# Kernel tuning notes

Measured on AMD Instinct MI355X. Metric: run time of the kernel, lower is better.

The kernel has to match this reference:

```python
import jax, jax.numpy as jnp
import numpy as np
from jax import lax

B, T, CIN, COUT, FACTOR = 2, 2048, 512, 512, 2
KUP = FACTOR * 2          # transposed-conv kernel
PUP = FACTOR // 2         # transposed-conv padding
KR, PR = 7, 3             # refine conv kernel/padding
EPS = 1e-5


def _ste(x, q):
    # straight-through estimator: forward = q, backward = identity
    return x + lax.stop_gradient(q - x)


def act_quant(x):
    # BitNet b1.58 per-token int8 absmax quant; x is (B, C, L), quant over C
    scale = 127.0 / jnp.maximum(jnp.max(jnp.abs(x), axis=1, keepdims=True), 1e-5)
    q = jnp.clip(jnp.round(x * scale), -128, 127) / scale
    return _ste(x, q)


def weight_quant(w):
    # ternary {-1,0,1} * scale, scale = mean |w|
    scale = 1.0 / jnp.maximum(jnp.mean(jnp.abs(w)), 1e-5)
    q = jnp.clip(jnp.round(w * scale), -1, 1) / scale
    return _ste(w, q)


def bit_conv1d(x, w, b, pad):
    # x: (B,C,L), w: (Cout,Cin,K) torch layout
    y = lax.conv_general_dilated(
        act_quant(x), weight_quant(w), window_strides=(1,),
        padding=[(pad, pad)], dimension_numbers=('NCH', 'OIH', 'NCH'))
    return y + b[None, :, None]


def bit_conv_transpose1d(x, w, b, stride, pad):
    # x: (B,Cin,L), w: (Cin,Cout,K) torch ConvTranspose1d layout
    k = w.shape[2]
    y = lax.conv_general_dilated(
        act_quant(x), jnp.flip(weight_quant(w), 2), window_strides=(1,),
        padding=[(k - 1 - pad, k - 1 - pad)], lhs_dilation=(stride,),
        dimension_numbers=('NCH', 'IOH', 'NCH'))
    return y + b[None, :, None]


def setup_inputs() -> dict:
    key = jax.random.key(0)
    ks = jax.random.split(key, 7)
    s_up = 1.0 / np.sqrt(CIN * KUP)
    s_r = 1.0 / np.sqrt(COUT * KR)
    return {
        'x': jax.random.normal(ks[0], (B, T, CIN), jnp.float32),
        'w_up': jax.random.normal(ks[1], (CIN, COUT, KUP), jnp.float32) * s_up,
        'b_up': jnp.zeros((COUT,), jnp.float32),
        'w_r1': jax.random.normal(ks[2], (COUT, COUT, KR), jnp.float32) * s_r,
        'b_r1': jnp.zeros((COUT,), jnp.float32),
        'w_r2': jax.random.normal(ks[3], (COUT, COUT, KR), jnp.float32) * s_r,
        'b_r2': jnp.zeros((COUT,), jnp.float32),
        'ln_w': jnp.ones((COUT,), jnp.float32),
        'ln_b': jnp.zeros((COUT,), jnp.float32),
    }


def reference(x, w_up, b_up, w_r1, b_r1, w_r2, b_r2, ln_w, ln_b):
    h = jnp.swapaxes(x, 1, 2)                                  # (B,Cin,T)
    h = bit_conv_transpose1d(h, w_up, b_up, FACTOR, PUP)       # (B,Cout,factor*T)
    r = bit_conv1d(h, w_r1, b_r1, PR)
    r = jax.nn.silu(r)
    r = bit_conv1d(r, w_r2, b_r2, PR)
    h = h + r
    h = jnp.swapaxes(h, 1, 2)                                  # (B,L,Cout)
    mu = jnp.mean(h, axis=-1, keepdims=True)
    var = jnp.mean(jnp.square(h - mu), axis=-1, keepdims=True)
    return (h - mu) * lax.rsqrt(var + EPS) * ln_w + ln_b
```

## Files before the change

### kernel.cpp

```cpp
#include <hip/hip_runtime.h>
#include <hip/hip_bf16.h>
#include <cstdint>
#include <cstddef>


#define B_ 2
#define T_ 2048
#define L_ 4096
#define C_ 512

static constexpr int NUP = 512 * 512 * 4;
static constexpr int NR  = 512 * 512 * 7;

using v4i  = __attribute__((ext_vector_type(4))) int;
using v16i = __attribute__((ext_vector_type(16))) int;

__device__ __forceinline__ void gl16(const void* g, void* l) {
  __builtin_amdgcn_global_load_lds((const __attribute__((address_space(1))) unsigned int*)g,
                                   (__attribute__((address_space(3))) unsigned int*)l,
                                   16, 0, 0);
}


__device__ inline float block_reduce_sum_256(float v) {
  #pragma unroll
  for (int off = 32; off > 0; off >>= 1) v += __shfl_down(v, off, 64);
  __shared__ float s[4];
  __syncthreads();
  if ((threadIdx.x & 63) == 0) s[threadIdx.x >> 6] = v;
  __syncthreads();
  return (s[0] + s[1]) + (s[2] + s[3]);
}

__global__ void abssum3_partial(const float* __restrict__ w0, const float* __restrict__ w1,
                                const float* __restrict__ w2, float* __restrict__ partial) {
  int y = blockIdx.y;
  const float* w = (y == 0) ? w0 : (y == 1) ? w1 : w2;
  int n = (y == 0) ? NUP : NR;
  int idx = blockIdx.x * 256 + threadIdx.x;
  float s = 0.f;
  for (int i = idx; i < n; i += gridDim.x * 256) s += fabsf(w[i]);
  s = block_reduce_sum_256(s);
  if (threadIdx.x == 0) partial[y * 256 + blockIdx.x] = s;
}

__global__ void abssum3_final(const float* __restrict__ partial, float* __restrict__ out) {
  int y = blockIdx.x;
  float v = partial[y * 256 + threadIdx.x];
  v = block_reduce_sum_256(v);
  if (threadIdx.x == 0) out[y] = v;
}

__global__ void tern_all_kernel(const float* __restrict__ wu, const float* __restrict__ w1,
                                const float* __restrict__ w2, int8_t* __restrict__ ou,
                                int8_t* __restrict__ o1, int8_t* __restrict__ o2,
                                const float* __restrict__ wsum) {
  int y = blockIdx.y;
  int idx = blockIdx.x * 256 + threadIdx.x;
  if (y == 0) {
    if (idx >= NUP) return;
    float mean = wsum[0] * (1.0f / (float)NUP);
    float scale = 1.0f / fmaxf(mean, 1e-5f);
    float t = rintf(wu[idx] * scale);
    t = fminf(fmaxf(t, -1.f), 1.f);
    int ci = idx >> 11;
    int co = (idx >> 2) & 511;
    int k = idx & 3;
    int ptap = (k == 3) ? 0 : (k == 1) ? 1 : (k == 2) ? 2 : 3;
    ou[(((size_t)ptap * 32 + (ci >> 4)) * 512 + co) * 16 + (ci & 15)] = (int8_t)t;
  } else {
    if (idx >= NR) return;
    const float* w = (y == 1) ? w1 : w2;
    int8_t* o = (y == 1) ? o1 : o2;
    float mean = wsum[y] * (1.0f / (float)NR);
    float scale = 1.0f / fmaxf(mean, 1e-5f);
    float t = rintf(w[idx] * scale);
    t = fminf(fmaxf(t, -1.f), 1.f);
    int co = idx / 3584;
    int rem = idx - co * 3584;
    int ci = rem / 7;
    int k = rem - ci * 7;
    o[(((size_t)k * 32 + (ci >> 4)) * 512 + co) * 16 + (ci & 15)] = (int8_t)t;
  }
}

__global__ void act_quant_kernel(const float* __restrict__ x, int8_t* __restrict__ qd,
                                 float* __restrict__ inv, int Lb, int lbsh, int LinH) {
  int tok = blockIdx.x;
  int b = tok >> lbsh;
  int t = tok & (Lb - 1);
  const float* row = x + (size_t)tok * C_;
  int tid = threadIdx.x;
  float v0 = row[tid];
  float v1 = row[tid + 256];
  float m = fmaxf(fabsf(v0), fabsf(v1));
  #pragma unroll
  for (int off = 32; off > 0; off >>= 1) m = fmaxf(m, __shfl_down(m, off, 64));
  __shared__ float s[4];
  __shared__ __align__(16) int8_t sq[512];
  if ((tid & 63) == 0) s[tid >> 6] = m;
  __syncthreads();
  m = fmaxf(fmaxf(s[0], s[1]), fmaxf(s[2], s[3]));
  float scale = 127.0f / fmaxf(m, 1e-5f);
  float q0 = fminf(fmaxf(rintf(v0 * scale), -128.f), 127.f);
  float q1 = fminf(fmaxf(rintf(v1 * scale), -128.f), 127.f);
  sq[tid] = (int8_t)q0;
  sq[tid + 256] = (int8_t)q1;
  __syncthreads();
  if (tid < 32)
    *(v4i*)(qd + ((size_t)(b * 32 + tid) * LinH + 8 + t) * 16) = *(const v4i*)(sq + tid * 16);
  if (tid == 0) inv[(size_t)b * LinH + 8 + t] = 1.0f / scale;
}

template<int NTAPS, bool CONVT, int EPI>
__global__ __launch_bounds__(512, 2)
void conv_fused(const int8_t* __restrict__ qin, const float* __restrict__ invp, int LinH,
                const int8_t* __restrict__ wq, const float* __restrict__ wsum, int widx,
                float wninv, const float* __restrict__ bias,
                float* __restrict__ hout,
                int8_t* __restrict__ qout, float* __restrict__ invout, int LoutH,
                const float* __restrict__ res, const float* __restrict__ g,
                const float* __restrict__ be, float* __restrict__ lnout, int Lout) {
  __shared__ __align__(16) int8_t sA[32 * 38 * 16];
  __shared__ float sInv[40];
  __shared__ float sRedA[8][32];
  __shared__ float sRedB[8][32];
  __shared__ float sS0[32];
  __shared__ float sS1[32];
  __shared__ __align__(16) int8_t sQ[32][512];

  const int tid = threadIdx.x;
  const int w = tid >> 6, lane = tid & 63, q = lane >> 5, l31 = lane & 31;
  const int t0 = blockIdx.x * 32;
  const int b = blockIdx.y;
  int s0 = -3;
  const int8_t* wq_p = wq;
  int parity = 0;
  if (CONVT) {
    parity = blockIdx.z;
    s0 = parity - 1;
    wq_p += (size_t)parity * 2 * 32 * 512 * 16;
  }
  const int8_t* qin_b = qin + (size_t)b * 32 * LinH * 16;
  const float* inv_b = invp + (size_t)b * LinH + 8;

  #pragma unroll
  for (int i = 0; i < 3; ++i) {
    int base = i * 512 + w * 64;
    if (base < 1216) {
      int u = base + lane;
      int kq = u / 38;
      int row = u - kq * 38;
      gl16(qin_b + ((size_t)kq * LinH + (size_t)(t0 + 5 + row)) * 16,
           sA + (size_t)base * 16);
    }
  }
  if (tid < 38) sInv[tid] = inv_b[t0 - 3 + tid];
  __syncthreads();

  float fs0[16], fs1[16];
  v16i acc0{}, acc1{};
  #pragma unroll
  for (int r = 0; r < 16; ++r) { fs0[r] = 0.f; fs1[r] = 0.f; acc0[r] = 0; acc1[r] = 0; }

  const int col0 = w * 64 + l31;
  const int8_t* wt_base = wq_p + ((size_t)q * 512 + (size_t)col0) * 16;

  #pragma unroll 1
  for (int tap = 0; tap < NTAPS; ++tap) {
    const int shift = s0 + tap;
    const int8_t* aP = sA + (((size_t)q * 38) + (size_t)(3 + shift + l31)) * 16;
    const int8_t* wt = wt_base + (size_t)tap * (32 * 512 * 16);
    #pragma unroll
    for (int ks = 0; ks < 16; ++ks) {
      v4i a  = *(const v4i*)(aP + (size_t)ks * (2 * 38 * 16));
      v4i b0 = *(const v4i*)(wt + (size_t)ks * 16384);
      v4i b1 = *(const v4i*)(wt + (size_t)ks * 16384 + 512);
      acc0 = __builtin_amdgcn_mfma_i32_32x32x32_i8(a, b0, acc0, 0, 0, 0);
      acc1 = __builtin_amdgcn_mfma_i32_32x32x32_i8(a, b1, acc1, 0, 0, 0);
    }
    #pragma unroll
    for (int r = 0; r < 16; ++r) {
      int ro = (r & 3) + 8 * (r >> 2) + 4 * q;
      float sc = sInv[3 + shift + ro];
      fs0[r] = fmaf((float)acc0[r], sc, fs0[r]);
      fs1[r] = fmaf((float)acc1[r], sc, fs1[r]);
      acc0[r] = 0; acc1[r] = 0;
    }
  }

  const float wdq = fmaxf(wsum[widx] * wninv, 1e-5f);
  const float bv0 = bias[col0], bv1 = bias[col0 + 32];
  #pragma unroll
  for (int r = 0; r < 16; ++r) {
    fs0[r] = fs0[r] * wdq + bv0;
    fs1[r] = fs1[r] * wdq + bv1;
  }

  if constexpr (EPI == 0) {
    #pragma unroll
    for (int r = 0; r < 16; ++r) {
      int ro = (r & 3) + 8 * (r >> 2) + 4 * q;
      size_t base = ((size_t)b * Lout + 2 * (size_t)(t0 + ro) + parity) * 512;
      hout[base + col0] = fs0[r];
      hout[base + col0 + 32] = fs1[r];
    }
  }
  if constexpr (EPI == 1) {
    #pragma unroll
    for (int r = 0; r < 16; ++r) {
      fs0[r] = fs0[r] / (1.0f + expf(-fs0[r]));
      fs1[r] = fs1[r] / (1.0f + expf(-fs1[r]));
    }
  }

  if constexpr (EPI <= 1) {
    #pragma unroll
    for (int r = 0; r < 16; ++r) {
      int ro = (r & 3) + 8 * (r >> 2) + 4 * q;
      float m = fmaxf(fabsf(fs0[r]), fabsf(fs1[r]));
      #pragma unroll
      for (int off = 16; off > 0; off >>= 1) m = fmaxf(m, __shfl_xor(m, off, 64));
      if (l31 == 0) sRedA[w][ro] = m;
    }
    __syncthreads();
    if (tid < 32) {
      float m = sRedA[0][tid];
      #pragma unroll
      for (int ww = 1; ww < 8; ++ww) m = fmaxf(m, sRedA[ww][tid]);
      float mm = fmaxf(m, 1e-5f);
      sS0[tid] = 127.0f / mm;
      int tok = CONVT ? (2 * (t0 + tid) + parity) : (t0 + tid);
      invout[(size_t)b * LoutH + 8 + tok] = mm * (1.0f / 127.0f);
    }
    __syncthreads();
    #pragma unroll
    for (int r = 0; r < 16; ++r) {
      int ro = (r & 3) + 8 * (r >> 2) + 4 * q;
      float sc = sS0[ro];
      float q0 = fminf(fmaxf(rintf(fs0[r] * sc), -128.f), 127.f);
      float q1 = fminf(fmaxf(rintf(fs1[r] * sc), -128.f), 127.f);
      sQ[ro][col0] = (int8_t)q0;
      sQ[ro][col0 + 32] = (int8_t)q1;
    }
    __syncthreads();
    #pragma unroll
    for (int it = 0; it < 2; ++it) {
      int u = it * 512 + tid;
      int row = u >> 5, unit = u & 31;
      int tok = CONVT ? (2 * (t0 + row) + parity) : (t0 + row);
      *(v4i*)(qout + (((size_t)b * 32 + unit) * LoutH + 8 + tok) * 16) =
          *(const v4i*)(&sQ[row][unit * 16]);
    }
  } else {
    #pragma unroll
    for (int r = 0; r < 16; ++r) {
      int ro = (r & 3) + 8 * (r >> 2) + 4 * q;
      size_t base = ((size_t)b * Lout + (size_t)(t0 + ro)) * 512;
      fs0[r] += res[base + col0];
      fs1[r] += res[base + col0 + 32];
    }
    #pragma unroll
    for (int r = 0; r < 16; ++r) {
      int ro = (r & 3) + 8 * (r >> 2) + 4 * q;
      float s = fs0[r] + fs1[r];
      #pragma unroll
      for (int off = 16; off > 0; off >>= 1) s += __shfl_xor(s, off, 64);
      if (l31 == 0) sRedA[w][ro] = s;
    }
    __syncthreads();
    if (tid < 32) {
      float s = sRedA[0][tid];
      #pragma unroll
      for (int ww = 1; ww < 8; ++ww) s += sRedA[ww][tid];
      sS0[tid] = s * (1.0f / 512.0f);
    }
    __syncthreads();
    #pragma unroll
    for (int r = 0; r < 16; ++r) {
      int ro = (r & 3) + 8 * (r >> 2) + 4 * q;
      float mu = sS0[ro];
      float d0 = fs0[r] - mu, d1 = fs1[r] - mu;
      float ss = d0 * d0 + d1 * d1;
      #pragma unroll
      for (int off = 16; off > 0; off >>= 1) ss += __shfl_xor(ss, off, 64);
      if (l31 == 0) sRedB[w][ro] = ss;
    }
    __syncthreads();
    if (tid < 32) {
      float ssum = sRedB[0][tid];
      #pragma unroll
      for (int ww = 1; ww < 8; ++ww) ssum += sRedB[ww][tid];
      float var = ssum * (1.0f / 512.0f);
      sS1[tid] = 1.0f / sqrtf(var + 1e-5f);
    }
    __syncthreads();
    const float g0 = g[col0], g1 = g[col0 + 32];
    const float e0 = be[col0], e1 = be[col0 + 32];
    #pragma unroll
    for (int r = 0; r < 16; ++r) {
      int ro = (r & 3) + 8 * (r >> 2) + 4 * q;
      float mu = sS0[ro], rs = sS1[ro];
      size_t base = ((size_t)b * Lout + (size_t)(t0 + ro)) * 512;
      lnout[base + col0]      = (fs0[r] - mu) * rs * g0 + e0;
      lnout[base + col0 + 32] = (fs1[r] - mu) * rs * g1 + e1;
    }
  }
}


extern "C" void kernel_launch(void* const* d_in, const int* in_sizes, int n_in,
                              void* d_out, int out_size, void* d_ws, size_t ws_size,
                              hipStream_t stream) {
  const float* x    = (const float*)d_in[0];
  const float* w_up = (const float*)d_in[1];
  const float* b_up = (const float*)d_in[2];
  const float* w_r1 = (const float*)d_in[3];
  const float* b_r1 = (const float*)d_in[4];
  const float* w_r2 = (const float*)d_in[5];
  const float* b_r2 = (const float*)d_in[6];
  const float* ln_w = (const float*)d_in[7];
  const float* ln_b = (const float*)d_in[8];
  float* out = (float*)d_out;

  const int LXH = T_ + 16;
  const int LHH = L_ + 16;

  char* ws = (char*)d_ws;
  size_t off = 0;
  auto alloc = [&](size_t sz) { size_t p = off; off += (sz + 255) & ~(size_t)255; return p; };
  float*  wsum  = (float*) (ws + alloc(256));
  int8_t* qx    = (int8_t*)(ws + alloc((size_t)B_ * 32 * LXH * 16));
  int8_t* qh    = (int8_t*)(ws + alloc((size_t)B_ * 32 * LHH * 16));
  int8_t* qh2   = (int8_t*)(ws + alloc((size_t)B_ * 32 * LHH * 16));
  float*  invx  = (float*) (ws + alloc((size_t)B_ * LXH * 4));
  float*  invh  = (float*) (ws + alloc((size_t)B_ * LHH * 4));
  float*  invh2 = (float*) (ws + alloc((size_t)B_ * LHH * 4));
  size_t zero_bytes = off;
  float*  partial = (float*)(ws + alloc(3 * 256 * 4));
  int8_t* wqup = (int8_t*)(ws + alloc((size_t)4 * 32 * 512 * 16));
  int8_t* wq1  = (int8_t*)(ws + alloc((size_t)7 * 32 * 512 * 16));
  int8_t* wq2  = (int8_t*)(ws + alloc((size_t)7 * 32 * 512 * 16));
  float*  h    = (float*) (ws + alloc((size_t)B_ * L_ * C_ * 4));

  hipMemsetAsync(ws, 0, zero_bytes, stream);

  abssum3_partial<<<dim3(256, 3), 256, 0, stream>>>(w_up, w_r1, w_r2, partial);
  abssum3_final<<<3, 256, 0, stream>>>(partial, wsum);
  tern_all_kernel<<<dim3(NR / 256, 3), 256, 0, stream>>>(w_up, w_r1, w_r2,
                                                         wqup, wq1, wq2, wsum);

  act_quant_kernel<<<B_ * T_, 256, 0, stream>>>(x, qx, invx, T_, 11, LXH);

  conv_fused<2, true, 0><<<dim3(64, B_, 2), 512, 0, stream>>>(
      qx, invx, LXH, wqup, wsum, 0, 1.0f / (float)NUP, b_up,
      h, qh, invh, LHH, nullptr, nullptr, nullptr, nullptr, L_);

  conv_fused<7, false, 1><<<dim3(128, B_, 1), 512, 0, stream>>>(
      qh, invh, LHH, wq1, wsum, 1, 1.0f / (float)NR, b_r1,
      nullptr, qh2, invh2, LHH, nullptr, nullptr, nullptr, nullptr, L_);

  conv_fused<7, false, 2><<<dim3(128, B_, 1), 512, 0, stream>>>(
      qh2, invh2, LHH, wq2, wsum, 2, 1.0f / (float)NR, b_r2,
      nullptr, nullptr, nullptr, 0, h, ln_w, ln_b, out, L_);
}
```

Before: 227.8 us.

## Switch conv kernels to 16x16x64 int8 MFMA with 16-token tiles and 1024 threads

The fused conv kernels move from 32x32x32 int8 MFMA on 32-token tiles with 8 waves to 16x16x64 int8 MFMA on 16-token tiles with 16 waves of 32 output channels each. This doubles the grid and cuts per-thread accumulator registers, so more blocks can be resident to fill the GPU and hide the latency of streaming weights from global memory. In exchange, each weight byte is reused over only 16 tokens instead of 32, which doubles total weight traffic from L2, and the 1024-thread blocks pay more for their barriers.

```diff
diff --git a/kernel.cpp b/kernel.cpp
--- a/kernel.cpp
+++ b/kernel.cpp
@@ -13,7 +13,6 @@
 static constexpr int NR  = 512 * 512 * 7;
 
 using v4i  = __attribute__((ext_vector_type(4))) int;
-using v16i = __attribute__((ext_vector_type(16))) int;
 
 __device__ __forceinline__ void gl16(const void* g, void* l) {
   __builtin_amdgcn_global_load_lds((const __attribute__((address_space(1))) unsigned int*)g,
@@ -113,7 +112,7 @@
 }
 
 template<int NTAPS, bool CONVT, int EPI>
-__global__ __launch_bounds__(512, 2)
+__global__ __launch_bounds__(1024, 8)
 void conv_fused(const int8_t* __restrict__ qin, const float* __restrict__ invp, int LinH,
                 const int8_t* __restrict__ wq, const float* __restrict__ wsum, int widx,
                 float wninv, const float* __restrict__ bias,
@@ -121,17 +120,18 @@
                 int8_t* __restrict__ qout, float* __restrict__ invout, int LoutH,
                 const float* __restrict__ res, const float* __restrict__ g,
                 const float* __restrict__ be, float* __restrict__ lnout, int Lout) {
-  __shared__ __align__(16) int8_t sA[32 * 38 * 16];
-  __shared__ float sInv[40];
-  __shared__ float sRedA[8][32];
-  __shared__ float sRedB[8][32];
-  __shared__ float sS0[32];
-  __shared__ float sS1[32];
-  __shared__ __align__(16) int8_t sQ[32][512];
+  __shared__ __align__(16) int8_t sA[32 * 22 * 16];
+  __shared__ float sInv[24];
+  __shared__ float sRedA[16][16];
+  __shared__ float sRedB[16][16];
+  __shared__ float sS0[16];
+  __shared__ float sS1[16];
+  __shared__ __align__(16) int8_t sQ[16][512];
 
   const int tid = threadIdx.x;
-  const int w = tid >> 6, lane = tid & 63, q = lane >> 5, l31 = lane & 31;
-  const int t0 = blockIdx.x * 32;
+  const int w = tid >> 6, lane = tid & 63;
+  const int l15 = lane & 15, l4 = lane >> 4;
+  const int t0 = blockIdx.x * 16;
   const int b = blockIdx.y;
   int s0 = -3;
   const int8_t* wq_p = wq;
@@ -144,45 +144,44 @@
   const int8_t* qin_b = qin + (size_t)b * 32 * LinH * 16;
   const float* inv_b = invp + (size_t)b * LinH + 8;
 
-  #pragma unroll
-  for (int i = 0; i < 3; ++i) {
-    int base = i * 512 + w * 64;
-    if (base < 1216) {
+  {
+    int base = w * 64;
+    if (base < 704) {
       int u = base + lane;
-      int kq = u / 38;
-      int row = u - kq * 38;
+      int kq = u / 22;
+      int row = u - kq * 22;
       gl16(qin_b + ((size_t)kq * LinH + (size_t)(t0 + 5 + row)) * 16,
            sA + (size_t)base * 16);
     }
   }
-  if (tid < 38) sInv[tid] = inv_b[t0 - 3 + tid];
-  __syncthreads();
-
-  float fs0[16], fs1[16];
-  v16i acc0{}, acc1{};
+  if (tid < 22) sInv[tid] = inv_b[t0 - 3 + tid];
+  __syncthreads();
+
+  float fs0[4], fs1[4];
+  v4i acc0{}, acc1{};
   #pragma unroll
-  for (int r = 0; r < 16; ++r) { fs0[r] = 0.f; fs1[r] = 0.f; acc0[r] = 0; acc1[r] = 0; }
-
-  const int col0 = w * 64 + l31;
-  const int8_t* wt_base = wq_p + ((size_t)q * 512 + (size_t)col0) * 16;
+  for (int r = 0; r < 4; ++r) { fs0[r] = 0.f; fs1[r] = 0.f; acc0[r] = 0; acc1[r] = 0; }
+
+  const int c0 = w * 32;
+  const int8_t* wb = wq_p + ((size_t)l4 * 512 + (size_t)(c0 + l15)) * 16;
+  const int8_t* aB = sA + (size_t)l4 * (22 * 16);
 
   #pragma unroll 1
   for (int tap = 0; tap < NTAPS; ++tap) {
     const int shift = s0 + tap;
-    const int8_t* aP = sA + (((size_t)q * 38) + (size_t)(3 + shift + l31)) * 16;
-    const int8_t* wt = wt_base + (size_t)tap * (32 * 512 * 16);
-    #pragma unroll
-    for (int ks = 0; ks < 16; ++ks) {
-      v4i a  = *(const v4i*)(aP + (size_t)ks * (2 * 38 * 16));
-      v4i b0 = *(const v4i*)(wt + (size_t)ks * 16384);
-      v4i b1 = *(const v4i*)(wt + (size_t)ks * 16384 + 512);
-      acc0 = __builtin_amdgcn_mfma_i32_32x32x32_i8(a, b0, acc0, 0, 0, 0);
-      acc1 = __builtin_amdgcn_mfma_i32_32x32x32_i8(a, b1, acc1, 0, 0, 0);
-    }
-    #pragma unroll
-    for (int r = 0; r < 16; ++r) {
-      int ro = (r & 3) + 8 * (r >> 2) + 4 * q;
-      float sc = sInv[3 + shift + ro];
+    const int8_t* aP = aB + (size_t)(3 + shift + l15) * 16;
+    const int8_t* wt = wb + (size_t)tap * (32 * 512 * 16);
+    #pragma unroll
+    for (int kc = 0; kc < 8; ++kc) {
+      v4i a  = *(const v4i*)(aP + (size_t)kc * (4 * 22 * 16));
+      v4i b0 = *(const v4i*)(wt + (size_t)kc * 32768);
+      v4i b1 = *(const v4i*)(wt + (size_t)kc * 32768 + 256);
+      acc0 = __builtin_amdgcn_mfma_i32_16x16x64_i8(a, b0, acc0, 0, 0, 0);
+      acc1 = __builtin_amdgcn_mfma_i32_16x16x64_i8(a, b1, acc1, 0, 0, 0);
+    }
+    #pragma unroll
+    for (int r = 0; r < 4; ++r) {
+      float sc = sInv[3 + shift + l4 * 4 + r];
       fs0[r] = fmaf((float)acc0[r], sc, fs0[r]);
       fs1[r] = fmaf((float)acc1[r], sc, fs1[r]);
       acc0[r] = 0; acc1[r] = 0;
@@ -190,25 +189,26 @@
   }
 
   const float wdq = fmaxf(wsum[widx] * wninv, 1e-5f);
-  const float bv0 = bias[col0], bv1 = bias[col0 + 32];
+  const float bv0 = bias[c0 + l15];
+  const float bv1 = bias[c0 + 16 + l15];
   #pragma unroll
-  for (int r = 0; r < 16; ++r) {
+  for (int r = 0; r < 4; ++r) {
     fs0[r] = fs0[r] * wdq + bv0;
     fs1[r] = fs1[r] * wdq + bv1;
   }
 
   if constexpr (EPI == 0) {
     #pragma unroll
-    for (int r = 0; r < 16; ++r) {
-      int ro = (r & 3) + 8 * (r >> 2) + 4 * q;
-      size_t base = ((size_t)b * Lout + 2 * (size_t)(t0 + ro) + parity) * 512;
-      hout[base + col0] = fs0[r];
-      hout[base + col0 + 32] = fs1[r];
+    for (int r = 0; r < 4; ++r) {
+      int m = l4 * 4 + r;
+      size_t base = ((size_t)b * Lout + 2 * (size_t)(t0 + m) + parity) * 512;
+      hout[base + c0 + l15] = fs0[r];
+      hout[base + c0 + 16 + l15] = fs1[r];
     }
   }
   if constexpr (EPI == 1) {
     #pragma unroll
-    for (int r = 0; r < 16; ++r) {
+    for (int r = 0; r < 4; ++r) {
       fs0[r] = fs0[r] / (1.0f + expf(-fs0[r]));
       fs1[r] = fs1[r] / (1.0f + expf(-fs1[r]));
     }
@@ -216,94 +216,92 @@
 
   if constexpr (EPI <= 1) {
     #pragma unroll
-    for (int r = 0; r < 16; ++r) {
-      int ro = (r & 3) + 8 * (r >> 2) + 4 * q;
-      float m = fmaxf(fabsf(fs0[r]), fabsf(fs1[r]));
-      #pragma unroll
-      for (int off = 16; off > 0; off >>= 1) m = fmaxf(m, __shfl_xor(m, off, 64));
-      if (l31 == 0) sRedA[w][ro] = m;
-    }
-    __syncthreads();
-    if (tid < 32) {
-      float m = sRedA[0][tid];
-      #pragma unroll
-      for (int ww = 1; ww < 8; ++ww) m = fmaxf(m, sRedA[ww][tid]);
-      float mm = fmaxf(m, 1e-5f);
+    for (int r = 0; r < 4; ++r) {
+      int m = l4 * 4 + r;
+      float mv = fmaxf(fabsf(fs0[r]), fabsf(fs1[r]));
+      #pragma unroll
+      for (int off = 8; off > 0; off >>= 1) mv = fmaxf(mv, __shfl_xor(mv, off, 64));
+      if (l15 == 0) sRedA[w][m] = mv;
+    }
+    __syncthreads();
+    if (tid < 16) {
+      float mval = sRedA[0][tid];
+      #pragma unroll
+      for (int ww = 1; ww < 16; ++ww) mval = fmaxf(mval, sRedA[ww][tid]);
+      float mm = fmaxf(mval, 1e-5f);
       sS0[tid] = 127.0f / mm;
       int tok = CONVT ? (2 * (t0 + tid) + parity) : (t0 + tid);
       invout[(size_t)b * LoutH + 8 + tok] = mm * (1.0f / 127.0f);
     }
     __syncthreads();
     #pragma unroll
-    for (int r = 0; r < 16; ++r) {
-      int ro = (r & 3) + 8 * (r >> 2) + 4 * q;
-      float sc = sS0[ro];
+    for (int r = 0; r < 4; ++r) {
+      int m = l4 * 4 + r;
+      float sc = sS0[m];
       float q0 = fminf(fmaxf(rintf(fs0[r] * sc), -128.f), 127.f);
       float q1 = fminf(fmaxf(rintf(fs1[r] * sc), -128.f), 127.f);
-      sQ[ro][col0] = (int8_t)q0;
-      sQ[ro][col0 + 32] = (int8_t)q1;
-    }
-    __syncthreads();
-    #pragma unroll
-    for (int it = 0; it < 2; ++it) {
-      int u = it * 512 + tid;
-      int row = u >> 5, unit = u & 31;
+      sQ[m][c0 + l15] = (int8_t)q0;
+      sQ[m][c0 + 16 + l15] = (int8_t)q1;
+    }
+    __syncthreads();
+    if (tid < 512) {
+      int row = tid >> 5, unit = tid & 31;
       int tok = CONVT ? (2 * (t0 + row) + parity) : (t0 + row);
       *(v4i*)(qout + (((size_t)b * 32 + unit) * LoutH + 8 + tok) * 16) =
           *(const v4i*)(&sQ[row][unit * 16]);
     }
   } else {
     #pragma unroll
-    for (int r = 0; r < 16; ++r) {
-      int ro = (r & 3) + 8 * (r >> 2) + 4 * q;
-      size_t base = ((size_t)b * Lout + (size_t)(t0 + ro)) * 512;
-      fs0[r] += res[base + col0];
-      fs1[r] += res[base + col0 + 32];
-    }
-    #pragma unroll
-    for (int r = 0; r < 16; ++r) {
-      int ro = (r & 3) + 8 * (r >> 2) + 4 * q;
+    for (int r = 0; r < 4; ++r) {
+      int m = l4 * 4 + r;
+      size_t base = ((size_t)b * Lout + (size_t)(t0 + m)) * 512;
+      fs0[r] += res[base + c0 + l15];
+      fs1[r] += res[base + c0 + 16 + l15];
+    }
+    #pragma unroll
+    for (int r = 0; r < 4; ++r) {
+      int m = l4 * 4 + r;
       float s = fs0[r] + fs1[r];
       #pragma unroll
-      for (int off = 16; off > 0; off >>= 1) s += __shfl_xor(s, off, 64);
-      if (l31 == 0) sRedA[w][ro] = s;
-    }
-    __syncthreads();
-    if (tid < 32) {
+      for (int off = 8; off > 0; off >>= 1) s += __shfl_xor(s, off, 64);
+      if (l15 == 0) sRedA[w][m] = s;
+    }
+    __syncthreads();
+    if (tid < 16) {
       float s = sRedA[0][tid];
       #pragma unroll
-      for (int ww = 1; ww < 8; ++ww) s += sRedA[ww][tid];
+      for (int ww = 1; ww < 16; ++ww) s += sRedA[ww][tid];
       sS0[tid] = s * (1.0f / 512.0f);
     }
     __syncthreads();
     #pragma unroll
-    for (int r = 0; r < 16; ++r) {
-      int ro = (r & 3) + 8 * (r >> 2) + 4 * q;
-      float mu = sS0[ro];
+    for (int r = 0; r < 4; ++r) {
+      int m = l4 * 4 + r;
+      float mu = sS0[m];
       float d0 = fs0[r] - mu, d1 = fs1[r] - mu;
       float ss = d0 * d0 + d1 * d1;
       #pragma unroll
-      for (int off = 16; off > 0; off >>= 1) ss += __shfl_xor(ss, off, 64);
-      if (l31 == 0) sRedB[w][ro] = ss;
-    }
-    __syncthreads();
-    if (tid < 32) {
+      for (int off = 8; off > 0; off >>= 1) ss += __shfl_xor(ss, off, 64);
+      if (l15 == 0) sRedB[w][m] = ss;
+    }
+    __syncthreads();
+    if (tid < 16) {
       float ssum = sRedB[0][tid];
       #pragma unroll
-      for (int ww = 1; ww < 8; ++ww) ssum += sRedB[ww][tid];
+      for (int ww = 1; ww < 16; ++ww) ssum += sRedB[ww][tid];
       float var = ssum * (1.0f / 512.0f);
       sS1[tid] = 1.0f / sqrtf(var + 1e-5f);
     }
     __syncthreads();
-    const float g0 = g[col0], g1 = g[col0 + 32];
-    const float e0 = be[col0], e1 = be[col0 + 32];
-    #pragma unroll
-    for (int r = 0; r < 16; ++r) {
-      int ro = (r & 3) + 8 * (r >> 2) + 4 * q;
-      float mu = sS0[ro], rs = sS1[ro];
-      size_t base = ((size_t)b * Lout + (size_t)(t0 + ro)) * 512;
-      lnout[base + col0]      = (fs0[r] - mu) * rs * g0 + e0;
-      lnout[base + col0 + 32] = (fs1[r] - mu) * rs * g1 + e1;
+    const float g0 = g[c0 + l15], g1 = g[c0 + 16 + l15];
+    const float e0 = be[c0 + l15], e1 = be[c0 + 16 + l15];
+    #pragma unroll
+    for (int r = 0; r < 4; ++r) {
+      int m = l4 * 4 + r;
+      float mu = sS0[m], rs = sS1[m];
+      size_t base = ((size_t)b * Lout + (size_t)(t0 + m)) * 512;
+      lnout[base + c0 + l15]      = (fs0[r] - mu) * rs * g0 + e0;
+      lnout[base + c0 + 16 + l15] = (fs1[r] - mu) * rs * g1 + e1;
     }
   }
 }
@@ -352,15 +350,15 @@
 
   act_quant_kernel<<<B_ * T_, 256, 0, stream>>>(x, qx, invx, T_, 11, LXH);
 
-  conv_fused<2, true, 0><<<dim3(64, B_, 2), 512, 0, stream>>>(
+  conv_fused<2, true, 0><<<dim3(T_ / 16, B_, 2), 1024, 0, stream>>>(
       qx, invx, LXH, wqup, wsum, 0, 1.0f / (float)NUP, b_up,
       h, qh, invh, LHH, nullptr, nullptr, nullptr, nullptr, L_);
 
-  conv_fused<7, false, 1><<<dim3(128, B_, 1), 512, 0, stream>>>(
+  conv_fused<7, false, 1><<<dim3(L_ / 16, B_, 1), 1024, 0, stream>>>(
       qh, invh, LHH, wq1, wsum, 1, 1.0f / (float)NR, b_r1,
       nullptr, qh2, invh2, LHH, nullptr, nullptr, nullptr, nullptr, L_);
 
-  conv_fused<7, false, 2><<<dim3(128, B_, 1), 512, 0, stream>>>(
+  conv_fused<7, false, 2><<<dim3(L_ / 16, B_, 1), 1024, 0, stream>>>(
       qh2, invh2, LHH, wq2, wsum, 2, 1.0f / (float)NR, b_r2,
       nullptr, nullptr, nullptr, 0, h, ln_w, ln_b, out, L_);
 }
```

New measurement: 214.8 us. 1.06x faster.
